# Optimization experiments

Hardware: AMD Instinct MI355X
Metric: run time of the kernel (lower is better)

The kernel has to match this reference:

```python
import jax, jax.numpy as jnp
import numpy as np

EPS = 1e-5

def lin(x, w, b):
    # torch nn.Linear convention: w [out,in]
    return x @ w.T + b

def bn(x, g, b):
    # nn.BatchNorm1d(element_num) on [B,N,C]: channels = dim 1 (N), stats over (B,C), training mode
    m = x.mean(axis=(0, 2), keepdims=True)
    v = x.var(axis=(0, 2), keepdims=True)
    return (x - m) / jnp.sqrt(v + EPS) * g[None, :, None] + b[None, :, None]

def relmod(x, wu, bu, ps, ph, wr):
    # Vectorized form of the triple loop:
    # f'_i = wr * (sum_{j!=i} (psi*phi)*<x_i,x_j> * relu(unary(x_j))) / N + x_i
    n = x.shape[1]
    U = jax.nn.relu(x @ wu.T + bu)                       # [B,N,D]
    S = (ps[0] * ph[0]) * jnp.einsum('bnd,bmd->bnm', x, x)  # [B,N,N]
    S = S * (1.0 - jnp.eye(n, dtype=x.dtype))            # exclude j == i
    return wr[0] * (jnp.einsum('bnm,bmd->bnd', S, U) / n) + x

def fwd(x, fc1_w, fc1_b, bn1_g, bn1_b, fc2_w, fc2_b, bn2_g, bn2_b, fc3_w, fc3_b,
        u1_w, u1_b, ps1, ph1, wr1, u2_w, u2_b, ps2, ph2, wr2,
        u3_w, u3_b, ps3, ph3, wr3, u4_w, u4_b, ps4, ph4, wr4,
        fc4_w, fc4_b, bn4_g, bn4_b, fc5_w, fc5_b, fc6_w, fc6_b, fc7_w, fc7_b):
    out = jax.nn.relu(bn(lin(x, fc1_w, fc1_b), bn1_g, bn1_b))
    out = jax.nn.relu(bn(lin(out, fc2_w, fc2_b), bn2_g, bn2_b))
    enc = jax.nn.sigmoid(lin(out, fc3_w, fc3_b))
    r = relmod(enc, u1_w, u1_b, ps1, ph1, wr1)
    r = relmod(r, u2_w, u2_b, ps2, ph2, wr2)
    r = relmod(r, u3_w, u3_b, ps3, ph3, wr3)
    r = relmod(r, u4_w, u4_b, ps4, ph4, wr4)
    out = jax.nn.relu(bn(lin(r, fc4_w, fc4_b), bn4_g, bn4_b))
    out = jax.nn.relu(lin(out, fc5_w, fc5_b))
    cls = lin(out, fc6_w, fc6_b)
    geo = lin(out, fc7_w, fc7_b)
    return jnp.concatenate([cls, geo], axis=2)

def setup_inputs() -> dict:
    B, N, F = 16, 2048, 3
    D2, D4 = 2 * F, 4 * F
    key = jax.random.key(0)
    ks = iter(jax.random.split(key, 64))
    nk = lambda: next(ks)
    W = lambda o, i: (jax.random.normal(nk(), (o, i), jnp.float32) / np.sqrt(i)).astype(jnp.float32)
    bv = lambda o: jnp.zeros((o,), jnp.float32)
    sc = lambda: jax.random.uniform(nk(), (1,), jnp.float32)
    inp = {'x': jax.random.normal(nk(), (B, N, F), jnp.float32)}
    inp.update(fc1_w=W(D2, F), fc1_b=bv(D2), bn1_g=jnp.ones((N,), jnp.float32), bn1_b=bv(N))
    inp.update(fc2_w=W(D4, D2), fc2_b=bv(D4), bn2_g=jnp.ones((N,), jnp.float32), bn2_b=bv(N))
    inp.update(fc3_w=W(D4, D4), fc3_b=bv(D4))
    inp.update(u1_w=W(D4, D4), u1_b=bv(D4), ps1=sc(), ph1=sc(), wr1=sc())
    inp.update(u2_w=W(D4, D4), u2_b=bv(D4), ps2=sc(), ph2=sc(), wr2=sc())
    inp.update(u3_w=W(D4, D4), u3_b=bv(D4), ps3=sc(), ph3=sc(), wr3=sc())
    inp.update(u4_w=W(D4, D4), u4_b=bv(D4), ps4=sc(), ph4=sc(), wr4=sc())
    inp.update(fc4_w=W(D2, D4), fc4_b=bv(D2), bn4_g=jnp.ones((N,), jnp.float32), bn4_b=bv(N))
    inp.update(fc5_w=W(F, D2), fc5_b=bv(F))
    inp.update(fc6_w=W(1, F), fc6_b=bv(1))
    inp.update(fc7_w=W(F - 1, F), fc7_b=bv(F - 1))
    return inp

def reference(x, fc1_w, fc1_b, bn1_g, bn1_b, fc2_w, fc2_b, bn2_g, bn2_b, fc3_w, fc3_b,
              u1_w, u1_b, ps1, ph1, wr1, u2_w, u2_b, ps2, ph2, wr2,
              u3_w, u3_b, ps3, ph3, wr3, u4_w, u4_b, ps4, ph4, wr4,
              fc4_w, fc4_b, bn4_g, bn4_b, fc5_w, fc5_b, fc6_w, fc6_b, fc7_w, fc7_b):
    return fwd(x, fc1_w, fc1_b, bn1_g, bn1_b, fc2_w, fc2_b, bn2_g, bn2_b, fc3_w, fc3_b,
               u1_w, u1_b, ps1, ph1, wr1, u2_w, u2_b, ps2, ph2, wr2,
               u3_w, u3_b, ps3, ph3, wr3, u4_w, u4_b, ps4, ph4, wr4,
               fc4_w, fc4_b, bn4_g, bn4_b, fc5_w, fc5_b, fc6_w, fc6_b, fc7_w, fc7_b)
```

## Files before the change

kernel.cpp:

```cpp
#include <hip/hip_runtime.h>
#include <math.h>

#define NB    16
#define NPTS  2048
#define DDIM  12
#define CHUNK 128
#define NCH   16
#define LPAD  132

__global__ __launch_bounds__(128) void k1_encode(
    const float* __restrict__ x,
    const float* __restrict__ fc1_w, const float* __restrict__ fc1_b,
    const float* __restrict__ bn1_g, const float* __restrict__ bn1_b,
    const float* __restrict__ fc2_w, const float* __restrict__ fc2_b,
    const float* __restrict__ bn2_g, const float* __restrict__ bn2_b,
    const float* __restrict__ fc3_w, const float* __restrict__ fc3_b,
    float* __restrict__ enc)
{
    __shared__ float w1[18], b1[6], w2[72], b2[12], w3[144], b3[12];
    const int tid = threadIdx.x;
    for (int k = tid; k < 144; k += 128) w3[k] = fc3_w[k];
    if (tid < 18) w1[tid] = fc1_w[tid];
    if (tid < 6)  b1[tid] = fc1_b[tid];
    if (tid < 72) w2[tid] = fc2_w[tid];
    if (tid < 12) { b2[tid] = fc2_b[tid]; b3[tid] = fc3_b[tid]; }
    __syncthreads();

    const int b  = tid & 15;
    const int nl = tid >> 4;
    const int n  = blockIdx.x * 8 + nl;

    const float* xp = x + (b * NPTS + n) * 3;
    const float x0 = xp[0], x1 = xp[1], x2 = xp[2];

    float h1[6];
    float s = 0.f, q = 0.f;
#pragma unroll
    for (int c = 0; c < 6; ++c) {
        float h = fmaf(w1[c*3+0], x0, fmaf(w1[c*3+1], x1, fmaf(w1[c*3+2], x2, b1[c])));
        h1[c] = h; s += h; q = fmaf(h, h, q);
    }
#pragma unroll
    for (int m = 1; m <= 8; m <<= 1) { s += __shfl_xor(s, m); q += __shfl_xor(q, m); }
    const float m1 = s * (1.f/96.f);
    const float i1 = 1.f / sqrtf(q*(1.f/96.f) - m1*m1 + 1e-5f);
    const float g1 = bn1_g[n], e1 = bn1_b[n];
    float a1[6];
#pragma unroll
    for (int c = 0; c < 6; ++c) a1[c] = fmaxf((h1[c] - m1) * i1 * g1 + e1, 0.f);

    float h2[12];
    s = 0.f; q = 0.f;
#pragma unroll
    for (int c = 0; c < 12; ++c) {
        float h = b2[c];
#pragma unroll
        for (int d = 0; d < 6; ++d) h = fmaf(w2[c*6+d], a1[d], h);
        h2[c] = h; s += h; q = fmaf(h, h, q);
    }
#pragma unroll
    for (int m = 1; m <= 8; m <<= 1) { s += __shfl_xor(s, m); q += __shfl_xor(q, m); }
    const float m2 = s * (1.f/192.f);
    const float i2 = 1.f / sqrtf(q*(1.f/192.f) - m2*m2 + 1e-5f);
    const float g2 = bn2_g[n], e2 = bn2_b[n];
    float a2[12];
#pragma unroll
    for (int c = 0; c < 12; ++c) a2[c] = fmaxf((h2[c] - m2) * i2 * g2 + e2, 0.f);

    float* ep = enc + (b * NPTS + n) * DDIM;
#pragma unroll
    for (int c = 0; c < 12; ++c) {
        float h = b3[c];
#pragma unroll
        for (int d = 0; d < 12; ++d) h = fmaf(w3[c*12+d], a2[d], h);
        ep[c] = 1.f / (1.f + expf(-h));
    }
}

__device__ __forceinline__ void reduce_partial(
    const float* xT, const float* uT, int tid, float* __restrict__ Pout, int bidx)
{
    if (tid < 144) {
        const int d = tid / 12;
        const int e = tid - d * 12;
        const float4* xp = (const float4*)(xT + d * LPAD);
        const float4* up = (const float4*)(uT + e * LPAD);
        float m = 0.f;
#pragma unroll
        for (int r = 0; r < CHUNK/4; ++r) {
            float4 a = xp[r], c = up[r];
            m = fmaf(a.x, c.x, m); m = fmaf(a.y, c.y, m);
            m = fmaf(a.z, c.z, m); m = fmaf(a.w, c.w, m);
        }
        Pout[bidx * 144 + tid] = m;
    }
}

__global__ __launch_bounds__(256) void k_reduce(
    const float* __restrict__ xb,
    const float* __restrict__ uw, const float* __restrict__ ub,
    float* __restrict__ Pout)
{
    __shared__ float W[144], B[12];
    __shared__ float xT[DDIM * LPAD], uT[DDIM * LPAD];
    const int tid = threadIdx.x;
    const int batch = blockIdx.x >> 4, ch = blockIdx.x & 15;
    for (int k = tid; k < 144; k += 256) W[k] = uw[k];
    if (tid < 12) B[tid] = ub[tid];
    __syncthreads();

    if (tid < CHUNK) {
        const float* row = xb + ((batch * NPTS) + ch * CHUNK + tid) * DDIM;
        float xr[12];
#pragma unroll
        for (int d = 0; d < 12; ++d) xr[d] = row[d];
#pragma unroll
        for (int k = 0; k < 12; ++k) {
            float a = B[k];
#pragma unroll
            for (int d = 0; d < 12; ++d) a = fmaf(W[k*12+d], xr[d], a);
            uT[k * LPAD + tid] = fmaxf(a, 0.f);
            xT[k * LPAD + tid] = xr[k];
        }
    }
    __syncthreads();
    reduce_partial(xT, uT, tid, Pout, blockIdx.x);
}

__global__ __launch_bounds__(256) void k_apply_reduce(
    float* __restrict__ xb,
    const float* __restrict__ Pin, float* __restrict__ Pout,
    const float* __restrict__ wc, const float* __restrict__ bc,
    const float* __restrict__ ps, const float* __restrict__ ph, const float* __restrict__ wr,
    const float* __restrict__ wn, const float* __restrict__ bn)
{
    __shared__ float Wc[144], Bc[12], Wn[144], Bn[12], Ml[144];
    __shared__ float xT[DDIM * LPAD], uT[DDIM * LPAD];
    const int tid = threadIdx.x;
    const int batch = blockIdx.x >> 4, ch = blockIdx.x & 15;
    for (int k = tid; k < 144; k += 256) { Wc[k] = wc[k]; Wn[k] = wn[k]; }
    if (tid < 12) { Bc[tid] = bc[tid]; Bn[tid] = bn[tid]; }
    if (tid < 144) {
        float sm = 0.f;
#pragma unroll
        for (int c = 0; c < NCH; ++c) sm += Pin[(batch * NCH + c) * 144 + tid];
        Ml[tid] = sm;
    }
    __syncthreads();

    const float coef = wr[0] * ps[0] * ph[0] * (1.f / (float)NPTS);
    if (tid < CHUNK) {
        float* rowp = xb + ((batch * NPTS) + ch * CHUNK + tid) * DDIM;
        float xr[12];
#pragma unroll
        for (int d = 0; d < 12; ++d) xr[d] = rowp[d];
        float uc[12];
#pragma unroll
        for (int k = 0; k < 12; ++k) {
            float a = Bc[k];
#pragma unroll
            for (int d = 0; d < 12; ++d) a = fmaf(Wc[k*12+d], xr[d], a);
            uc[k] = fmaxf(a, 0.f);
        }
        float xx = 0.f;
#pragma unroll
        for (int d = 0; d < 12; ++d) xx = fmaf(xr[d], xr[d], xx);
        float fo[12];
#pragma unroll
        for (int e = 0; e < 12; ++e) {
            float acc = 0.f;
#pragma unroll
            for (int d = 0; d < 12; ++d) acc = fmaf(xr[d], Ml[d*12+e], acc);
            fo[e] = fmaf(coef, fmaf(-xx, uc[e], acc), xr[e]);
        }
#pragma unroll
        for (int e = 0; e < 12; ++e) rowp[e] = fo[e];
#pragma unroll
        for (int k = 0; k < 12; ++k) {
            float a = Bn[k];
#pragma unroll
            for (int d = 0; d < 12; ++d) a = fmaf(Wn[k*12+d], fo[d], a);
            uT[k * LPAD + tid] = fmaxf(a, 0.f);
            xT[k * LPAD + tid] = fo[k];
        }
    }
    __syncthreads();
    reduce_partial(xT, uT, tid, Pout, blockIdx.x);
}

__global__ __launch_bounds__(128) void k3_head(
    const float* __restrict__ xb, const float* __restrict__ P4,
    const float* __restrict__ u4w, const float* __restrict__ u4b,
    const float* __restrict__ ps4, const float* __restrict__ ph4, const float* __restrict__ wr4,
    const float* __restrict__ fc4_w, const float* __restrict__ fc4_b,
    const float* __restrict__ bn4_g, const float* __restrict__ bn4_b,
    const float* __restrict__ fc5_w, const float* __restrict__ fc5_b,
    const float* __restrict__ fc6_w, const float* __restrict__ fc6_b,
    const float* __restrict__ fc7_w, const float* __restrict__ fc7_b,
    float* __restrict__ out)
{
    __shared__ float W4[144], B4[12], M4[NB * 144];
    __shared__ float w4[72], b4[6], w5[18], b5[3], w6[3], w7[6], bb[3];
    const int tid = threadIdx.x;
    for (int k = tid; k < 144; k += 128) W4[k] = u4w[k];
    if (tid < 12) B4[tid] = u4b[tid];
    for (int k = tid; k < NB * 144; k += 128) {
        const int bt = k / 144, ix = k - bt * 144;
        float sm = 0.f;
#pragma unroll
        for (int c = 0; c < NCH; ++c) sm += P4[(bt * NCH + c) * 144 + ix];
        M4[k] = sm;
    }
    if (tid < 72) w4[tid] = fc4_w[tid];
    if (tid < 6)  b4[tid] = fc4_b[tid];
    if (tid < 18) w5[tid] = fc5_w[tid];
    if (tid < 3)  { b5[tid] = fc5_b[tid]; w6[tid] = fc6_w[tid]; }
    if (tid < 6)  w7[tid] = fc7_w[tid];
    if (tid == 0) bb[0] = fc6_b[0];
    if (tid < 2)  bb[1 + tid] = fc7_b[tid];
    __syncthreads();

    const int b  = tid & 15;
    const int nl = tid >> 4;
    const int n  = blockIdx.x * 8 + nl;
    const float coef = wr4[0] * ps4[0] * ph4[0] * (1.f / (float)NPTS);

    const float* rowp = xb + (b * NPTS + n) * DDIM;
    float xr[12];
#pragma unroll
    for (int d = 0; d < 12; ++d) xr[d] = rowp[d];
    float uc[12];
#pragma unroll
    for (int k = 0; k < 12; ++k) {
        float a = B4[k];
#pragma unroll
        for (int d = 0; d < 12; ++d) a = fmaf(W4[k*12+d], xr[d], a);
        uc[k] = fmaxf(a, 0.f);
    }
    float xx = 0.f;
#pragma unroll
    for (int d = 0; d < 12; ++d) xx = fmaf(xr[d], xr[d], xx);
    const float* Mb = M4 + b * 144;
    float r4[12];
#pragma unroll
    for (int e = 0; e < 12; ++e) {
        float acc = 0.f;
#pragma unroll
        for (int d = 0; d < 12; ++d) acc = fmaf(xr[d], Mb[d*12+e], acc);
        r4[e] = fmaf(coef, fmaf(-xx, uc[e], acc), xr[e]);
    }

    float h4[6];
    float s = 0.f, q = 0.f;
#pragma unroll
    for (int c = 0; c < 6; ++c) {
        float h = b4[c];
#pragma unroll
        for (int d = 0; d < 12; ++d) h = fmaf(w4[c*12+d], r4[d], h);
        h4[c] = h; s += h; q = fmaf(h, h, q);
    }
#pragma unroll
    for (int m = 1; m <= 8; m <<= 1) { s += __shfl_xor(s, m); q += __shfl_xor(q, m); }
    const float mm = s * (1.f/96.f);
    const float iv = 1.f / sqrtf(q*(1.f/96.f) - mm*mm + 1e-5f);
    const float g4 = bn4_g[n], e4 = bn4_b[n];
    float a4[6];
#pragma unroll
    for (int c = 0; c < 6; ++c) a4[c] = fmaxf((h4[c] - mm) * iv * g4 + e4, 0.f);

    float a5[3];
#pragma unroll
    for (int c = 0; c < 3; ++c) {
        float h = b5[c];
#pragma unroll
        for (int d = 0; d < 6; ++d) h = fmaf(w5[c*6+d], a4[d], h);
        a5[c] = fmaxf(h, 0.f);
    }
    const float cls = fmaf(w6[0], a5[0], fmaf(w6[1], a5[1], fmaf(w6[2], a5[2], bb[0])));
    const float g0  = fmaf(w7[0], a5[0], fmaf(w7[1], a5[1], fmaf(w7[2], a5[2], bb[1])));
    const float g1v = fmaf(w7[3], a5[0], fmaf(w7[4], a5[1], fmaf(w7[5], a5[2], bb[2])));
    float* op = out + (b * NPTS + n) * 3;
    op[0] = cls; op[1] = g0; op[2] = g1v;
}

extern "C" void kernel_launch(void* const* d_in, const int* in_sizes, int n_in,
                              void* d_out, int out_size, void* d_ws, size_t ws_size,
                              hipStream_t stream)
{
    const float* X = (const float*)d_in[0];
    float* enc = (float*)d_ws;
    float* Pa  = enc + NB * NPTS * DDIM;
    float* Pb  = Pa + NB * NCH * 144;

    k1_encode<<<NPTS/8, 128, 0, stream>>>(
        X,
        (const float*)d_in[1],  (const float*)d_in[2],
        (const float*)d_in[3],  (const float*)d_in[4],
        (const float*)d_in[5],  (const float*)d_in[6],
        (const float*)d_in[7],  (const float*)d_in[8],
        (const float*)d_in[9],  (const float*)d_in[10],
        enc);

    k_reduce<<<NB*NCH, 256, 0, stream>>>(
        enc, (const float*)d_in[11], (const float*)d_in[12], Pa);

    k_apply_reduce<<<NB*NCH, 256, 0, stream>>>(
        enc, Pa, Pb,
        (const float*)d_in[11], (const float*)d_in[12],
        (const float*)d_in[13], (const float*)d_in[14], (const float*)d_in[15],
        (const float*)d_in[16], (const float*)d_in[17]);

    k_apply_reduce<<<NB*NCH, 256, 0, stream>>>(
        enc, Pb, Pa,
        (const float*)d_in[16], (const float*)d_in[17],
        (const float*)d_in[18], (const float*)d_in[19], (const float*)d_in[20],
        (const float*)d_in[21], (const float*)d_in[22]);

    k_apply_reduce<<<NB*NCH, 256, 0, stream>>>(
        enc, Pa, Pb,
        (const float*)d_in[21], (const float*)d_in[22],
        (const float*)d_in[23], (const float*)d_in[24], (const float*)d_in[25],
        (const float*)d_in[26], (const float*)d_in[27]);

    k3_head<<<NPTS/8, 128, 0, stream>>>(
        enc, Pb,
        (const float*)d_in[26], (const float*)d_in[27],
        (const float*)d_in[28], (const float*)d_in[29], (const float*)d_in[30],
        (const float*)d_in[31], (const float*)d_in[32],
        (const float*)d_in[33], (const float*)d_in[34],
        (const float*)d_in[35], (const float*)d_in[36],
        (const float*)d_in[37], (const float*)d_in[38],
        (const float*)d_in[39], (const float*)d_in[40],
        (float*)d_out);
}
```

Before: 170.1 us.

## Fuse whole forward pass into one cooperative kernel with grid syncs

Replaces the six separate launches (encode, reduce, three apply-reduce, head) with one cooperative kernel of 256 blocks that keeps each point's 12-dim row in registers across all four relation stages, using grid.sync between stages. Each thread recomputes the first two encoder layers for all 16 batches of its point, so the batch-norm stats come out locally without a cross-block step. The final batch norm's statistics go through a small global buffer plus another grid sync. This removes launch overhead and the global round trips of the intermediate activations, at the cost of grid-wide barriers, redundant encoder compute and a dependence on every block being co-resident.

```diff
diff --git a/kernel.cpp b/kernel.cpp
--- a/kernel.cpp
+++ b/kernel.cpp
@@ -1,272 +1,260 @@
 #include <hip/hip_runtime.h>
+#include <hip/hip_cooperative_groups.h>
 #include <math.h>
+
+namespace cg = cooperative_groups;
 
 #define NB    16
 #define NPTS  2048
-#define DDIM  12
+#define NROW  (NB * NPTS)
 #define CHUNK 128
 #define NCH   16
 #define LPAD  132
 
-__global__ __launch_bounds__(128) void k1_encode(
-    const float* __restrict__ x,
-    const float* __restrict__ fc1_w, const float* __restrict__ fc1_b,
-    const float* __restrict__ bn1_g, const float* __restrict__ bn1_b,
-    const float* __restrict__ fc2_w, const float* __restrict__ fc2_b,
-    const float* __restrict__ bn2_g, const float* __restrict__ bn2_b,
-    const float* __restrict__ fc3_w, const float* __restrict__ fc3_b,
-    float* __restrict__ enc)
+struct KArgs {
+    const float *x;
+    const float *fc1_w, *fc1_b, *bn1_g, *bn1_b;
+    const float *fc2_w, *fc2_b, *bn2_g, *bn2_b;
+    const float *fc3_w, *fc3_b;
+    const float *uw0, *ub0, *ps0, *ph0, *wr0;
+    const float *uw1, *ub1, *ps1, *ph1, *wr1;
+    const float *uw2, *ub2, *ps2, *ph2, *wr2;
+    const float *uw3, *ub3, *ps3, *ph3, *wr3;
+    const float *fc4_w, *fc4_b, *bn4_g, *bn4_b;
+    const float *fc5_w, *fc5_b, *fc6_w, *fc6_b, *fc7_w, *fc7_b;
+    float2 *G;
+    float  *Pa, *Pb;
+    float  *out;
+};
+
+__device__ __forceinline__ void block_dots(const float* xT, const float* uT,
+                                           int tid, float* __restrict__ Pout, int blk)
 {
-    __shared__ float w1[18], b1[6], w2[72], b2[12], w3[144], b3[12];
-    const int tid = threadIdx.x;
-    for (int k = tid; k < 144; k += 128) w3[k] = fc3_w[k];
-    if (tid < 18) w1[tid] = fc1_w[tid];
-    if (tid < 6)  b1[tid] = fc1_b[tid];
-    if (tid < 72) w2[tid] = fc2_w[tid];
-    if (tid < 12) { b2[tid] = fc2_b[tid]; b3[tid] = fc3_b[tid]; }
-    __syncthreads();
-
-    const int b  = tid & 15;
-    const int nl = tid >> 4;
-    const int n  = blockIdx.x * 8 + nl;
-
-    const float* xp = x + (b * NPTS + n) * 3;
-    const float x0 = xp[0], x1 = xp[1], x2 = xp[2];
-
-    float h1[6];
-    float s = 0.f, q = 0.f;
-#pragma unroll
-    for (int c = 0; c < 6; ++c) {
-        float h = fmaf(w1[c*3+0], x0, fmaf(w1[c*3+1], x1, fmaf(w1[c*3+2], x2, b1[c])));
-        h1[c] = h; s += h; q = fmaf(h, h, q);
-    }
-#pragma unroll
-    for (int m = 1; m <= 8; m <<= 1) { s += __shfl_xor(s, m); q += __shfl_xor(q, m); }
-    const float m1 = s * (1.f/96.f);
-    const float i1 = 1.f / sqrtf(q*(1.f/96.f) - m1*m1 + 1e-5f);
-    const float g1 = bn1_g[n], e1 = bn1_b[n];
-    float a1[6];
-#pragma unroll
-    for (int c = 0; c < 6; ++c) a1[c] = fmaxf((h1[c] - m1) * i1 * g1 + e1, 0.f);
-
-    float h2[12];
-    s = 0.f; q = 0.f;
-#pragma unroll
-    for (int c = 0; c < 12; ++c) {
-        float h = b2[c];
-#pragma unroll
-        for (int d = 0; d < 6; ++d) h = fmaf(w2[c*6+d], a1[d], h);
-        h2[c] = h; s += h; q = fmaf(h, h, q);
-    }
-#pragma unroll
-    for (int m = 1; m <= 8; m <<= 1) { s += __shfl_xor(s, m); q += __shfl_xor(q, m); }
-    const float m2 = s * (1.f/192.f);
-    const float i2 = 1.f / sqrtf(q*(1.f/192.f) - m2*m2 + 1e-5f);
-    const float g2 = bn2_g[n], e2 = bn2_b[n];
-    float a2[12];
-#pragma unroll
-    for (int c = 0; c < 12; ++c) a2[c] = fmaxf((h2[c] - m2) * i2 * g2 + e2, 0.f);
-
-    float* ep = enc + (b * NPTS + n) * DDIM;
-#pragma unroll
-    for (int c = 0; c < 12; ++c) {
-        float h = b3[c];
-#pragma unroll
-        for (int d = 0; d < 12; ++d) h = fmaf(w3[c*12+d], a2[d], h);
-        ep[c] = 1.f / (1.f + expf(-h));
-    }
-}
-
-__device__ __forceinline__ void reduce_partial(
-    const float* xT, const float* uT, int tid, float* __restrict__ Pout, int bidx)
-{
-    if (tid < 144) {
-        const int d = tid / 12;
-        const int e = tid - d * 12;
+    for (int k = tid; k < 144; k += CHUNK) {
+        const int d = k / 12, e = k - d * 12;
         const float4* xp = (const float4*)(xT + d * LPAD);
         const float4* up = (const float4*)(uT + e * LPAD);
         float m = 0.f;
 #pragma unroll
-        for (int r = 0; r < CHUNK/4; ++r) {
-            float4 a = xp[r], c = up[r];
-            m = fmaf(a.x, c.x, m); m = fmaf(a.y, c.y, m);
-            m = fmaf(a.z, c.z, m); m = fmaf(a.w, c.w, m);
-        }
-        Pout[bidx * 144 + tid] = m;
+        for (int r = 0; r < CHUNK / 4; ++r) {
+            float4 A = xp[r], C = up[r];
+            m = fmaf(A.x, C.x, m); m = fmaf(A.y, C.y, m);
+            m = fmaf(A.z, C.z, m); m = fmaf(A.w, C.w, m);
+        }
+        Pout[blk * 144 + k] = m;
     }
 }
 
-__global__ __launch_bounds__(256) void k_reduce(
-    const float* __restrict__ xb,
-    const float* __restrict__ uw, const float* __restrict__ ub,
-    float* __restrict__ Pout)
+__global__ __launch_bounds__(128) void fused_all(KArgs a)
 {
-    __shared__ float W[144], B[12];
-    __shared__ float xT[DDIM * LPAD], uT[DDIM * LPAD];
-    const int tid = threadIdx.x;
-    const int batch = blockIdx.x >> 4, ch = blockIdx.x & 15;
-    for (int k = tid; k < 144; k += 256) W[k] = uw[k];
-    if (tid < 12) B[tid] = ub[tid];
+    __shared__ float w1[18], b1[6], w2[72], b2[12], w3[144], b3[12];
+    __shared__ float Wu[4][144], Bu[4][12];
+    __shared__ float w4[72], b4[6], w5[18], b5[3], w6[3], w7[6], hb[3];
+    __shared__ float xT[12 * LPAD], uT[12 * LPAD], Ml[144];
+
+    const int tid   = threadIdx.x;
+    const int blk   = blockIdx.x;
+    const int batch = blk >> 4, ch = blk & 15;
+    const int n     = ch * CHUNK + tid;
+    const int gRow  = batch * NPTS + n;
+
+    for (int k = tid; k < 144; k += 128) {
+        w3[k] = a.fc3_w[k];
+        Wu[0][k] = a.uw0[k]; Wu[1][k] = a.uw1[k];
+        Wu[2][k] = a.uw2[k]; Wu[3][k] = a.uw3[k];
+    }
+    if (tid < 18) { w1[tid] = a.fc1_w[tid]; w5[tid] = a.fc5_w[tid]; }
+    if (tid < 6)  { b1[tid] = a.fc1_b[tid]; b4[tid] = a.fc4_b[tid]; w7[tid] = a.fc7_w[tid]; }
+    if (tid < 72) { w2[tid] = a.fc2_w[tid]; w4[tid] = a.fc4_w[tid]; }
+    if (tid < 12) {
+        b2[tid] = a.fc2_b[tid]; b3[tid] = a.fc3_b[tid];
+        Bu[0][tid] = a.ub0[tid]; Bu[1][tid] = a.ub1[tid];
+        Bu[2][tid] = a.ub2[tid]; Bu[3][tid] = a.ub3[tid];
+    }
+    if (tid < 3)  { b5[tid] = a.fc5_b[tid]; w6[tid] = a.fc6_w[tid]; }
+    if (tid == 0) { hb[0] = a.fc6_b[0]; hb[1] = a.fc7_b[0]; hb[2] = a.fc7_b[1]; }
     __syncthreads();
 
-    if (tid < CHUNK) {
-        const float* row = xb + ((batch * NPTS) + ch * CHUNK + tid) * DDIM;
-        float xr[12];
-#pragma unroll
-        for (int d = 0; d < 12; ++d) xr[d] = row[d];
+    cg::grid_group grid = cg::this_grid();
+
+    float xs0[NB], xs1[NB], xs2[NB];
+#pragma unroll
+    for (int bb = 0; bb < NB; ++bb) {
+        const float* xp = a.x + (bb * NPTS + n) * 3;
+        xs0[bb] = xp[0]; xs1[bb] = xp[1]; xs2[bb] = xp[2];
+    }
+    float s = 0.f, q = 0.f;
+#pragma unroll
+    for (int bb = 0; bb < NB; ++bb)
+#pragma unroll
+        for (int c = 0; c < 6; ++c) {
+            float h = fmaf(w1[c*3], xs0[bb], fmaf(w1[c*3+1], xs1[bb], fmaf(w1[c*3+2], xs2[bb], b1[c])));
+            s += h; q = fmaf(h, h, q);
+        }
+    const float m1 = s * (1.f/96.f);
+    const float i1 = 1.f / sqrtf(q*(1.f/96.f) - m1*m1 + 1e-5f);
+    const float g1 = a.bn1_g[n] * i1, e1 = a.bn1_b[n];
+
+    float h2o[12];
+    s = 0.f; q = 0.f;
+#pragma unroll
+    for (int bb = 0; bb < NB; ++bb) {
+        float a1v[6];
+#pragma unroll
+        for (int c = 0; c < 6; ++c) {
+            float h = fmaf(w1[c*3], xs0[bb], fmaf(w1[c*3+1], xs1[bb], fmaf(w1[c*3+2], xs2[bb], b1[c])));
+            a1v[c] = fmaxf(fmaf(h - m1, g1, e1), 0.f);
+        }
+#pragma unroll
+        for (int c = 0; c < 12; ++c) {
+            float h = b2[c];
+#pragma unroll
+            for (int d = 0; d < 6; ++d) h = fmaf(w2[c*6+d], a1v[d], h);
+            s += h; q = fmaf(h, h, q);
+            if (bb == batch) h2o[c] = h;
+        }
+    }
+    const float m2 = s * (1.f/192.f);
+    const float i2 = 1.f / sqrtf(q*(1.f/192.f) - m2*m2 + 1e-5f);
+    const float g2 = a.bn2_g[n] * i2, e2 = a.bn2_b[n];
+
+    float a2[12];
+#pragma unroll
+    for (int c = 0; c < 12; ++c) a2[c] = fmaxf(fmaf(h2o[c] - m2, g2, e2), 0.f);
+
+    float row[12];
+#pragma unroll
+    for (int c = 0; c < 12; ++c) {
+        float h = b3[c];
+#pragma unroll
+        for (int d = 0; d < 12; ++d) h = fmaf(w3[c*12+d], a2[d], h);
+        row[c] = 1.f / (1.f + expf(-h));
+    }
+
+    {
+        float u[12];
 #pragma unroll
         for (int k = 0; k < 12; ++k) {
-            float a = B[k];
-#pragma unroll
-            for (int d = 0; d < 12; ++d) a = fmaf(W[k*12+d], xr[d], a);
-            uT[k * LPAD + tid] = fmaxf(a, 0.f);
-            xT[k * LPAD + tid] = xr[k];
-        }
-    }
-    __syncthreads();
-    reduce_partial(xT, uT, tid, Pout, blockIdx.x);
-}
-
-__global__ __launch_bounds__(256) void k_apply_reduce(
-    float* __restrict__ xb,
-    const float* __restrict__ Pin, float* __restrict__ Pout,
-    const float* __restrict__ wc, const float* __restrict__ bc,
-    const float* __restrict__ ps, const float* __restrict__ ph, const float* __restrict__ wr,
-    const float* __restrict__ wn, const float* __restrict__ bn)
-{
-    __shared__ float Wc[144], Bc[12], Wn[144], Bn[12], Ml[144];
-    __shared__ float xT[DDIM * LPAD], uT[DDIM * LPAD];
-    const int tid = threadIdx.x;
-    const int batch = blockIdx.x >> 4, ch = blockIdx.x & 15;
-    for (int k = tid; k < 144; k += 256) { Wc[k] = wc[k]; Wn[k] = wn[k]; }
-    if (tid < 12) { Bc[tid] = bc[tid]; Bn[tid] = bn[tid]; }
-    if (tid < 144) {
-        float sm = 0.f;
-#pragma unroll
-        for (int c = 0; c < NCH; ++c) sm += Pin[(batch * NCH + c) * 144 + tid];
-        Ml[tid] = sm;
-    }
-    __syncthreads();
-
-    const float coef = wr[0] * ps[0] * ph[0] * (1.f / (float)NPTS);
-    if (tid < CHUNK) {
-        float* rowp = xb + ((batch * NPTS) + ch * CHUNK + tid) * DDIM;
-        float xr[12];
-#pragma unroll
-        for (int d = 0; d < 12; ++d) xr[d] = rowp[d];
-        float uc[12];
+            float acc = Bu[0][k];
+#pragma unroll
+            for (int d = 0; d < 12; ++d) acc = fmaf(Wu[0][k*12+d], row[d], acc);
+            u[k] = fmaxf(acc, 0.f);
+        }
+#pragma unroll
+        for (int k = 0; k < 12; ++k) { xT[k*LPAD + tid] = row[k]; uT[k*LPAD + tid] = u[k]; }
+        __syncthreads();
+        block_dots(xT, uT, tid, a.Pa, blk);
+    }
+    grid.sync();
+
+#pragma unroll
+    for (int r = 0; r < 3; ++r) {
+        const float* Pin  = (r == 1) ? a.Pb : a.Pa;
+        float*       Pout = (r == 1) ? a.Pa : a.Pb;
+        const float* psp = (r == 0) ? a.ps0 : (r == 1) ? a.ps1 : a.ps2;
+        const float* php = (r == 0) ? a.ph0 : (r == 1) ? a.ph1 : a.ph2;
+        const float* wrp = (r == 0) ? a.wr0 : (r == 1) ? a.wr1 : a.wr2;
+        const float coef = wrp[0] * psp[0] * php[0] * (1.f / (float)NPTS);
+
+        for (int k = tid; k < 144; k += 128) {
+            float sm = 0.f;
+#pragma unroll
+            for (int c = 0; c < NCH; ++c) sm += Pin[(batch * NCH + c) * 144 + k];
+            Ml[k] = sm;
+        }
+        __syncthreads();
+
+        float u[12];
 #pragma unroll
         for (int k = 0; k < 12; ++k) {
-            float a = Bc[k];
-#pragma unroll
-            for (int d = 0; d < 12; ++d) a = fmaf(Wc[k*12+d], xr[d], a);
-            uc[k] = fmaxf(a, 0.f);
+            float acc = Bu[r][k];
+#pragma unroll
+            for (int d = 0; d < 12; ++d) acc = fmaf(Wu[r][k*12+d], row[d], acc);
+            u[k] = fmaxf(acc, 0.f);
         }
         float xx = 0.f;
 #pragma unroll
-        for (int d = 0; d < 12; ++d) xx = fmaf(xr[d], xr[d], xx);
+        for (int d = 0; d < 12; ++d) xx = fmaf(row[d], row[d], xx);
         float fo[12];
 #pragma unroll
         for (int e = 0; e < 12; ++e) {
             float acc = 0.f;
 #pragma unroll
-            for (int d = 0; d < 12; ++d) acc = fmaf(xr[d], Ml[d*12+e], acc);
-            fo[e] = fmaf(coef, fmaf(-xx, uc[e], acc), xr[e]);
-        }
-#pragma unroll
-        for (int e = 0; e < 12; ++e) rowp[e] = fo[e];
+            for (int d = 0; d < 12; ++d) acc = fmaf(row[d], Ml[d*12+e], acc);
+            fo[e] = fmaf(coef, fmaf(-xx, u[e], acc), row[e]);
+        }
+#pragma unroll
+        for (int d = 0; d < 12; ++d) row[d] = fo[d];
+
+        float un[12];
 #pragma unroll
         for (int k = 0; k < 12; ++k) {
-            float a = Bn[k];
-#pragma unroll
-            for (int d = 0; d < 12; ++d) a = fmaf(Wn[k*12+d], fo[d], a);
-            uT[k * LPAD + tid] = fmaxf(a, 0.f);
-            xT[k * LPAD + tid] = fo[k];
-        }
-    }
-    __syncthreads();
-    reduce_partial(xT, uT, tid, Pout, blockIdx.x);
-}
-
-__global__ __launch_bounds__(128) void k3_head(
-    const float* __restrict__ xb, const float* __restrict__ P4,
-    const float* __restrict__ u4w, const float* __restrict__ u4b,
-    const float* __restrict__ ps4, const float* __restrict__ ph4, const float* __restrict__ wr4,
-    const float* __restrict__ fc4_w, const float* __restrict__ fc4_b,
-    const float* __restrict__ bn4_g, const float* __restrict__ bn4_b,
-    const float* __restrict__ fc5_w, const float* __restrict__ fc5_b,
-    const float* __restrict__ fc6_w, const float* __restrict__ fc6_b,
-    const float* __restrict__ fc7_w, const float* __restrict__ fc7_b,
-    float* __restrict__ out)
-{
-    __shared__ float W4[144], B4[12], M4[NB * 144];
-    __shared__ float w4[72], b4[6], w5[18], b5[3], w6[3], w7[6], bb[3];
-    const int tid = threadIdx.x;
-    for (int k = tid; k < 144; k += 128) W4[k] = u4w[k];
-    if (tid < 12) B4[tid] = u4b[tid];
-    for (int k = tid; k < NB * 144; k += 128) {
-        const int bt = k / 144, ix = k - bt * 144;
-        float sm = 0.f;
-#pragma unroll
-        for (int c = 0; c < NCH; ++c) sm += P4[(bt * NCH + c) * 144 + ix];
-        M4[k] = sm;
-    }
-    if (tid < 72) w4[tid] = fc4_w[tid];
-    if (tid < 6)  b4[tid] = fc4_b[tid];
-    if (tid < 18) w5[tid] = fc5_w[tid];
-    if (tid < 3)  { b5[tid] = fc5_b[tid]; w6[tid] = fc6_w[tid]; }
-    if (tid < 6)  w7[tid] = fc7_w[tid];
-    if (tid == 0) bb[0] = fc6_b[0];
-    if (tid < 2)  bb[1 + tid] = fc7_b[tid];
-    __syncthreads();
-
-    const int b  = tid & 15;
-    const int nl = tid >> 4;
-    const int n  = blockIdx.x * 8 + nl;
-    const float coef = wr4[0] * ps4[0] * ph4[0] * (1.f / (float)NPTS);
-
-    const float* rowp = xb + (b * NPTS + n) * DDIM;
-    float xr[12];
-#pragma unroll
-    for (int d = 0; d < 12; ++d) xr[d] = rowp[d];
-    float uc[12];
-#pragma unroll
-    for (int k = 0; k < 12; ++k) {
-        float a = B4[k];
-#pragma unroll
-        for (int d = 0; d < 12; ++d) a = fmaf(W4[k*12+d], xr[d], a);
-        uc[k] = fmaxf(a, 0.f);
-    }
-    float xx = 0.f;
-#pragma unroll
-    for (int d = 0; d < 12; ++d) xx = fmaf(xr[d], xr[d], xx);
-    const float* Mb = M4 + b * 144;
-    float r4[12];
-#pragma unroll
-    for (int e = 0; e < 12; ++e) {
-        float acc = 0.f;
-#pragma unroll
-        for (int d = 0; d < 12; ++d) acc = fmaf(xr[d], Mb[d*12+e], acc);
-        r4[e] = fmaf(coef, fmaf(-xx, uc[e], acc), xr[e]);
+            float acc = Bu[r+1][k];
+#pragma unroll
+            for (int d = 0; d < 12; ++d) acc = fmaf(Wu[r+1][k*12+d], row[d], acc);
+            un[k] = fmaxf(acc, 0.f);
+        }
+        __syncthreads();
+#pragma unroll
+        for (int k = 0; k < 12; ++k) { xT[k*LPAD + tid] = row[k]; uT[k*LPAD + tid] = un[k]; }
+        __syncthreads();
+        block_dots(xT, uT, tid, Pout, blk);
+        grid.sync();
     }
 
     float h4[6];
-    float s = 0.f, q = 0.f;
-#pragma unroll
-    for (int c = 0; c < 6; ++c) {
-        float h = b4[c];
-#pragma unroll
-        for (int d = 0; d < 12; ++d) h = fmaf(w4[c*12+d], r4[d], h);
-        h4[c] = h; s += h; q = fmaf(h, h, q);
-    }
-#pragma unroll
-    for (int m = 1; m <= 8; m <<= 1) { s += __shfl_xor(s, m); q += __shfl_xor(q, m); }
-    const float mm = s * (1.f/96.f);
-    const float iv = 1.f / sqrtf(q*(1.f/96.f) - mm*mm + 1e-5f);
-    const float g4 = bn4_g[n], e4 = bn4_b[n];
+    {
+        for (int k = tid; k < 144; k += 128) {
+            float sm = 0.f;
+#pragma unroll
+            for (int c = 0; c < NCH; ++c) sm += a.Pb[(batch * NCH + c) * 144 + k];
+            Ml[k] = sm;
+        }
+        __syncthreads();
+        const float coef = a.wr3[0] * a.ps3[0] * a.ph3[0] * (1.f / (float)NPTS);
+        float u[12];
+#pragma unroll
+        for (int k = 0; k < 12; ++k) {
+            float acc = Bu[3][k];
+#pragma unroll
+            for (int d = 0; d < 12; ++d) acc = fmaf(Wu[3][k*12+d], row[d], acc);
+            u[k] = fmaxf(acc, 0.f);
+        }
+        float xx = 0.f;
+#pragma unroll
+        for (int d = 0; d < 12; ++d) xx = fmaf(row[d], row[d], xx);
+        float fo[12];
+#pragma unroll
+        for (int e = 0; e < 12; ++e) {
+            float acc = 0.f;
+#pragma unroll
+            for (int d = 0; d < 12; ++d) acc = fmaf(row[d], Ml[d*12+e], acc);
+            fo[e] = fmaf(coef, fmaf(-xx, u[e], acc), row[e]);
+        }
+#pragma unroll
+        for (int d = 0; d < 12; ++d) row[d] = fo[d];
+
+        float ss = 0.f, qq = 0.f;
+#pragma unroll
+        for (int c = 0; c < 6; ++c) {
+            float h = b4[c];
+#pragma unroll
+            for (int d = 0; d < 12; ++d) h = fmaf(w4[c*12+d], row[d], h);
+            h4[c] = h; ss += h; qq = fmaf(h, h, qq);
+        }
+        a.G[gRow] = make_float2(ss, qq);
+    }
+    grid.sync();
+
+    s = 0.f; q = 0.f;
+#pragma unroll
+    for (int bb = 0; bb < NB; ++bb) { float2 t = a.G[bb * NPTS + n]; s += t.x; q += t.y; }
+    const float m4 = s * (1.f/96.f);
+    const float i4 = 1.f / sqrtf(q*(1.f/96.f) - m4*m4 + 1e-5f);
+    const float g4 = a.bn4_g[n] * i4, e4 = a.bn4_b[n];
     float a4[6];
 #pragma unroll
-    for (int c = 0; c < 6; ++c) a4[c] = fmaxf((h4[c] - mm) * iv * g4 + e4, 0.f);
+    for (int c = 0; c < 6; ++c) a4[c] = fmaxf(fmaf(h4[c] - m4, g4, e4), 0.f);
 
     float a5[3];
 #pragma unroll
@@ -276,10 +264,10 @@
         for (int d = 0; d < 6; ++d) h = fmaf(w5[c*6+d], a4[d], h);
         a5[c] = fmaxf(h, 0.f);
     }
-    const float cls = fmaf(w6[0], a5[0], fmaf(w6[1], a5[1], fmaf(w6[2], a5[2], bb[0])));
-    const float g0  = fmaf(w7[0], a5[0], fmaf(w7[1], a5[1], fmaf(w7[2], a5[2], bb[1])));
-    const float g1v = fmaf(w7[3], a5[0], fmaf(w7[4], a5[1], fmaf(w7[5], a5[2], bb[2])));
-    float* op = out + (b * NPTS + n) * 3;
+    const float cls = fmaf(w6[0], a5[0], fmaf(w6[1], a5[1], fmaf(w6[2], a5[2], hb[0])));
+    const float g0  = fmaf(w7[0], a5[0], fmaf(w7[1], a5[1], fmaf(w7[2], a5[2], hb[1])));
+    const float g1v = fmaf(w7[3], a5[0], fmaf(w7[4], a5[1], fmaf(w7[5], a5[2], hb[2])));
+    float* op = a.out + gRow * 3;
     op[0] = cls; op[1] = g0; op[2] = g1v;
 }
 
@@ -287,49 +275,34 @@
                               void* d_out, int out_size, void* d_ws, size_t ws_size,
                               hipStream_t stream)
 {
-    const float* X = (const float*)d_in[0];
-    float* enc = (float*)d_ws;
-    float* Pa  = enc + NB * NPTS * DDIM;
-    float* Pb  = Pa + NB * NCH * 144;
-
-    k1_encode<<<NPTS/8, 128, 0, stream>>>(
-        X,
-        (const float*)d_in[1],  (const float*)d_in[2],
-        (const float*)d_in[3],  (const float*)d_in[4],
-        (const float*)d_in[5],  (const float*)d_in[6],
-        (const float*)d_in[7],  (const float*)d_in[8],
-        (const float*)d_in[9],  (const float*)d_in[10],
-        enc);
-
-    k_reduce<<<NB*NCH, 256, 0, stream>>>(
-        enc, (const float*)d_in[11], (const float*)d_in[12], Pa);
-
-    k_apply_reduce<<<NB*NCH, 256, 0, stream>>>(
-        enc, Pa, Pb,
-        (const float*)d_in[11], (const float*)d_in[12],
-        (const float*)d_in[13], (const float*)d_in[14], (const float*)d_in[15],
-        (const float*)d_in[16], (const float*)d_in[17]);
-
-    k_apply_reduce<<<NB*NCH, 256, 0, stream>>>(
-        enc, Pb, Pa,
-        (const float*)d_in[16], (const float*)d_in[17],
-        (const float*)d_in[18], (const float*)d_in[19], (const float*)d_in[20],
-        (const float*)d_in[21], (const float*)d_in[22]);
-
-    k_apply_reduce<<<NB*NCH, 256, 0, stream>>>(
-        enc, Pa, Pb,
-        (const float*)d_in[21], (const float*)d_in[22],
-        (const float*)d_in[23], (const float*)d_in[24], (const float*)d_in[25],
-        (const float*)d_in[26], (const float*)d_in[27]);
-
-    k3_head<<<NPTS/8, 128, 0, stream>>>(
-        enc, Pb,
-        (const float*)d_in[26], (const float*)d_in[27],
-        (const float*)d_in[28], (const float*)d_in[29], (const float*)d_in[30],
-        (const float*)d_in[31], (const float*)d_in[32],
-        (const float*)d_in[33], (const float*)d_in[34],
-        (const float*)d_in[35], (const float*)d_in[36],
-        (const float*)d_in[37], (const float*)d_in[38],
-        (const float*)d_in[39], (const float*)d_in[40],
-        (float*)d_out);
+    KArgs ka;
+    ka.x     = (const float*)d_in[0];
+    ka.fc1_w = (const float*)d_in[1];  ka.fc1_b = (const float*)d_in[2];
+    ka.bn1_g = (const float*)d_in[3];  ka.bn1_b = (const float*)d_in[4];
+    ka.fc2_w = (const float*)d_in[5];  ka.fc2_b = (const float*)d_in[6];
+    ka.bn2_g = (const float*)d_in[7];  ka.bn2_b = (const float*)d_in[8];
+    ka.fc3_w = (const float*)d_in[9];  ka.fc3_b = (const float*)d_in[10];
+    ka.uw0 = (const float*)d_in[11]; ka.ub0 = (const float*)d_in[12];
+    ka.ps0 = (const float*)d_in[13]; ka.ph0 = (const float*)d_in[14]; ka.wr0 = (const float*)d_in[15];
+    ka.uw1 = (const float*)d_in[16]; ka.ub1 = (const float*)d_in[17];
+    ka.ps1 = (const float*)d_in[18]; ka.ph1 = (const float*)d_in[19]; ka.wr1 = (const float*)d_in[20];
+    ka.uw2 = (const float*)d_in[21]; ka.ub2 = (const float*)d_in[22];
+    ka.ps2 = (const float*)d_in[23]; ka.ph2 = (const float*)d_in[24]; ka.wr2 = (const float*)d_in[25];
+    ka.uw3 = (const float*)d_in[26]; ka.ub3 = (const float*)d_in[27];
+    ka.ps3 = (const float*)d_in[28]; ka.ph3 = (const float*)d_in[29]; ka.wr3 = (const float*)d_in[30];
+    ka.fc4_w = (const float*)d_in[31]; ka.fc4_b = (const float*)d_in[32];
+    ka.bn4_g = (const float*)d_in[33]; ka.bn4_b = (const float*)d_in[34];
+    ka.fc5_w = (const float*)d_in[35]; ka.fc5_b = (const float*)d_in[36];
+    ka.fc6_w = (const float*)d_in[37]; ka.fc6_b = (const float*)d_in[38];
+    ka.fc7_w = (const float*)d_in[39]; ka.fc7_b = (const float*)d_in[40];
+
+    float* ws = (float*)d_ws;
+    ka.G  = (float2*)ws;
+    ka.Pa = ws + 65536;
+    ka.Pb = ws + 65536 + 36864;
+    ka.out = (float*)d_out;
+
+    void* args[] = { &ka };
+    hipLaunchCooperativeKernel((void*)fused_all, dim3(NB * NCH), dim3(CHUNK),
+                               args, 0, stream);
 }
```

Measured after the change: 353.4 us. 2.08x slower.
